# Kernel optimization log

Measured on AMD Instinct MI355X. Metric: run time of the kernel, lower is better.

The kernel has to match this reference:

```python
import jax, jax.numpy as jnp
import numpy as np

B = 65536
D = 512            # resnet18 fc.in_features
NUM_CLASSES = 512  # size of batch_centers
LEVELS = [2048, 1024, 512]


def setup_inputs() -> dict:
    key = jax.random.key(0)
    ks = jax.random.split(key, 8)
    x = jax.random.normal(ks[0], (B, D), dtype=jnp.float32)
    labels = jax.random.randint(ks[1], (B,), 0, NUM_CLASSES, dtype=jnp.int64)
    W0 = jax.random.normal(ks[2], (LEVELS[0], D), dtype=jnp.float32) * 0.02
    b0 = jnp.zeros((LEVELS[0],), dtype=jnp.float32)
    W1 = jax.random.normal(ks[3], (LEVELS[1], LEVELS[0]), dtype=jnp.float32) * 0.02
    b1 = jnp.zeros((LEVELS[1],), dtype=jnp.float32)
    W2 = jax.random.normal(ks[4], (LEVELS[2], LEVELS[1]), dtype=jnp.float32) * 0.02
    b2 = jnp.zeros((LEVELS[2],), dtype=jnp.float32)
    lambda_values = jnp.array([1e-3, 1.0, 1.0, 1.0], dtype=jnp.float32)
    return {"x": x, "W0": W0, "b0": b0, "W1": W1, "b1": b1,
            "W2": W2, "b2": b2, "lambda_values": lambda_values,
            "labels": labels}


def _cross_entropy(logits, labels):
    # mean over batch of -log p(label) (torch CrossEntropyLoss default)
    logp = jax.nn.log_softmax(logits, axis=-1)
    nll = -jnp.take_along_axis(logp, labels[:, None], axis=-1)[:, 0]
    return jnp.mean(nll)


def reference(x, W0, b0, W1, b1, W2, b2, lambda_values, labels):
    # --- per-class scatter-mean centers (vectorized segment reduce) ---
    sums = jax.ops.segment_sum(x, labels, num_segments=NUM_CLASSES)
    counts = jax.ops.segment_sum(jnp.ones((x.shape[0],), x.dtype), labels,
                                 num_segments=NUM_CLASSES)
    centers = jnp.where(counts[:, None] > 0,
                        sums / jnp.maximum(counts, 1.0)[:, None],
                        0.0)  # classes absent from batch keep zero centers
    # --- gather-diff center loss: sum_i ||x_i - c_{y_i}||^2 ---
    diff = x - centers[labels]
    center_loss = jnp.sum(diff * diff)
    # --- cascaded classification heads, CE at each level ---
    h = x
    losses = []
    for W, b in ((W0, b0), (W1, b1), (W2, b2)):
        h = h @ W.T + b
        losses.append(_cross_entropy(h, labels))
    classification_losses = jnp.stack(losses)
    return lambda_values[0] * center_loss + jnp.dot(lambda_values[1:],
                                                    classification_losses)
```

## Files before the change

### kernel.cpp

```cpp
#include <hip/hip_runtime.h>
#include <cstdint>
#include <cstddef>

using f32x4  = __attribute__((ext_vector_type(4))) float;
using i32x4v = __attribute__((ext_vector_type(4))) int;
using i32x8v = __attribute__((ext_vector_type(8))) int;

__device__ __forceinline__ unsigned char f2fp8(float f) {
  return (unsigned char)(__builtin_amdgcn_cvt_pk_fp8_f32(f, f, 0, false) & 0xff);
}

__device__ __forceinline__ float waveRed(float v) {
#pragma unroll
  for (int m = 32; m >= 1; m >>= 1) v += __shfl_xor(v, m, 64);
  return v;
}

__device__ __forceinline__ void gload16(const void* g, void* l) {
  __builtin_amdgcn_global_load_lds(
      (__attribute__((address_space(1))) uint32_t*)(uintptr_t)g,
      (__attribute__((address_space(3))) uint32_t*)(uint32_t*)l,
      16, 0, 0);
}

__global__ __launch_bounds__(256) void prep_w(
    const float4* __restrict__ W1, const float4* __restrict__ W2,
    const float4* __restrict__ W0f4, const float* __restrict__ W0,
    const float* __restrict__ b0,
    uint32_t* __restrict__ W1_8, uint32_t* __restrict__ W2_8,
    uint32_t* __restrict__ W0_8, unsigned char* __restrict__ W0t8,
    float* __restrict__ zr, int zwords, float* __restrict__ biascat) {
  __shared__ unsigned char t8[64][65];
  const int b = blockIdx.x;
  const int tid = threadIdx.x;
  if (b < 1024) {
    for (int i = b * 256 + tid; i < 524288; i += 1024 * 256) {
      float4 v = W1[i];
      int p = __builtin_amdgcn_cvt_pk_fp8_f32(v.x, v.y, 0, false);
      p = __builtin_amdgcn_cvt_pk_fp8_f32(v.z, v.w, p, true);
      W1_8[i] = (uint32_t)p;
    }
  } else if (b < 1280) {
    for (int i = (b - 1024) * 256 + tid; i < 131072; i += 256 * 256) {
      float4 v = W2[i];
      int p = __builtin_amdgcn_cvt_pk_fp8_f32(v.x, v.y, 0, false);
      p = __builtin_amdgcn_cvt_pk_fp8_f32(v.z, v.w, p, true);
      W2_8[i] = (uint32_t)p;
    }
  } else if (b < 1536) {
    for (int i = (b - 1280) * 256 + tid; i < 262144; i += 256 * 256) {
      float4 v = W0f4[i];
      int p = __builtin_amdgcn_cvt_pk_fp8_f32(v.x, v.y, 0, false);
      p = __builtin_amdgcn_cvt_pk_fp8_f32(v.z, v.w, p, true);
      W0_8[i] = (uint32_t)p;
    }
  } else if (b < 1792) {
    const int t = b - 1536;
    const int r0 = (t >> 3) * 64, c0 = (t & 7) * 64;
#pragma unroll
    for (int p = 0; p < 16; ++p) {
      const int row = p * 4 + (tid >> 6), col = tid & 63;
      t8[row][col] = f2fp8(W0[(size_t)(r0 + row) * 512 + c0 + col]);
    }
    __syncthreads();
#pragma unroll
    for (int p = 0; p < 16; ++p) {
      const int oc = p * 4 + (tid >> 6), orr = tid & 63;
      W0t8[(size_t)(c0 + oc) * 2048 + r0 + orr] = t8[orr][oc];
    }
  } else if (b < 2819) {
    const int i = (b - 1792) * 256 + tid;
    if (i < zwords) zr[i] = 0.f;
  } else {
    const int i = (b - 2819) * 256 + tid;
    if (i < 2048) biascat[i] = b0[i];
  }
}

__global__ __launch_bounds__(256) void count_k(const int* __restrict__ lab,
                                               int* __restrict__ counts, int n) {
  __shared__ int h[512];
  for (int i = threadIdx.x; i < 512; i += 256) h[i] = 0;
  __syncthreads();
  for (int i = blockIdx.x * 256 + threadIdx.x; i < n; i += gridDim.x * 256)
    atomicAdd(&h[lab[i]], 1);
  __syncthreads();
  for (int i = threadIdx.x; i < 512; i += 256) {
    int v = h[i];
    if (v) atomicAdd(&counts[i], v);
  }
}

__global__ void prefix_k(const int* __restrict__ counts, int* __restrict__ offsets,
                         int* __restrict__ cursor, int nc) {
  const int lane = threadIdx.x;
  int base = 0;
  for (int c0 = 0; c0 < nc; c0 += 64) {
    int v = counts[c0 + lane];
    int x = v;
#pragma unroll
    for (int d = 1; d < 64; d <<= 1) {
      int y = __shfl_up(x, d, 64);
      if (lane >= d) x += y;
    }
    int excl = base + x - v;
    offsets[c0 + lane] = excl;
    cursor[c0 + lane] = excl;
    base += __shfl(x, 63, 64);
  }
}

__global__ void scatter_k(const int* __restrict__ lab, int* __restrict__ cursor,
                          int* __restrict__ buckets, int n) {
  for (int i = blockIdx.x * 256 + threadIdx.x; i < n; i += gridDim.x * 256) {
    int pos = atomicAdd(&cursor[lab[i]], 1);
    buckets[pos] = i;
  }
}

__global__ __launch_bounds__(256) void csum_k(const float* __restrict__ x,
    const int* __restrict__ buckets, const int* __restrict__ offsets,
    const int* __restrict__ counts, float* __restrict__ centers) {
  const int c = blockIdx.x >> 2, q = blockIdx.x & 3;
  const int cnt = counts[c];
  if (cnt == 0) return;
  const int beg = offsets[c];
  const int lo = beg + (cnt * q) / 4, hi = beg + (cnt * (q + 1)) / 4;
  const int t = threadIdx.x;
  float sx = 0.f, sy = 0.f;
  for (int i = lo; i < hi; ++i) {
    const int row = buckets[i];
    const float2 v = ((const float2*)(x + (size_t)row * 512))[t];
    sx += v.x; sy += v.y;
  }
  if (lo < hi) {
    atomicAdd(&centers[c * 512 + 2 * t], sx);
    atomicAdd(&centers[c * 512 + 2 * t + 1], sy);
  }
}

__global__ __launch_bounds__(256) void cnorm_k(const float* __restrict__ centers,
    const int* __restrict__ counts, float* __restrict__ out) {
  const int c = blockIdx.x;
  const int cnt = counts[c];
  if (cnt == 0) return;
  const float2 v = ((const float2*)(centers + (size_t)c * 512))[threadIdx.x];
  float ssq = v.x * v.x + v.y * v.y;
  ssq = waveRed(ssq);
  __shared__ float red[4];
  if ((threadIdx.x & 63) == 0) red[threadIdx.x >> 6] = ssq;
  __syncthreads();
  if (threadIdx.x == 0)
    atomicAdd(out, (red[0] + red[1] + red[2] + red[3]) / (float)cnt);
}

__global__ __launch_bounds__(256) void matvec_k(const float* __restrict__ W,
    const float* __restrict__ vin, const float* __restrict__ badd,
    float* __restrict__ vout, int K) {
  int row = blockIdx.x;
  float s = 0.f;
  for (int k = threadIdx.x; k < K; k += 256) s += W[(size_t)row * K + k] * vin[k];
  s = waveRed(s);
  __shared__ float red[4];
  if ((threadIdx.x & 63) == 0) red[threadIdx.x >> 6] = s;
  __syncthreads();
  if (threadIdx.x == 0) vout[row] = red[0] + red[1] + red[2] + red[3] + badd[row];
}

__global__ __launch_bounds__(256) void gemm8_w(
    const unsigned char* __restrict__ A8, const unsigned char* __restrict__ B8,
    int M, int N, int K, unsigned char* __restrict__ C8,
    unsigned char* __restrict__ Ct8) {
  __shared__ __align__(16) unsigned char As[128 * 128];
  __shared__ __align__(16) unsigned char Bs[128 * 128];
  const int tid = threadIdx.x;
  const int lane = tid & 63;
  const int wave = tid >> 6;
  const int lane16 = lane & 15;
  const int quad = lane >> 4;
  const int wm = (wave >> 1) * 64;
  const int wn = (wave & 1) * 64;
  const int m0 = blockIdx.y * 128;
  const int n0 = blockIdx.x * 128;

  f32x4 acc[4][4] = {};

  int srow[4], goff[4];
#pragma unroll
  for (int q = 0; q < 4; ++q) {
    const int s = tid + q * 256;
    const int row = s >> 3;
    const int c16 = s & 7;
    srow[q] = row;
    goff[q] = (((c16 >> 1) ^ (row & 3)) << 5) + ((c16 & 1) << 4);
  }

  for (int kt = 0; kt < K; kt += 128) {
#pragma unroll
    for (int q = 0; q < 4; ++q) {
      const int s = tid + q * 256;
      gload16(A8 + (size_t)(m0 + srow[q]) * K + kt + goff[q], &As[s * 16]);
      gload16(B8 + (size_t)(n0 + srow[q]) * K + kt + goff[q], &Bs[s * 16]);
    }
    __syncthreads();
    i32x8v a8[4], b8[4];
#pragma unroll
    for (int i = 0; i < 4; ++i) {
      const int row = i * 16 + lane16;
      const int sc = quad ^ (row & 3);
      const unsigned char* pa = &As[row * 128 + sc * 32];
      const i32x4v lo = *(const i32x4v*)pa;
      const i32x4v hi = *(const i32x4v*)(pa + 16);
      a8[i] = (i32x8v){lo[0], lo[1], lo[2], lo[3], hi[0], hi[1], hi[2], hi[3]};
    }
#pragma unroll
    for (int j = 0; j < 4; ++j) {
      const int row = j * 16 + lane16;
      const int sc = quad ^ (row & 3);
      const unsigned char* pb = &Bs[row * 128 + sc * 32];
      const i32x4v lo = *(const i32x4v*)pb;
      const i32x4v hi = *(const i32x4v*)(pb + 16);
      b8[j] = (i32x8v){lo[0], lo[1], lo[2], lo[3], hi[0], hi[1], hi[2], hi[3]};
    }
#pragma unroll
    for (int i = 0; i < 4; ++i)
#pragma unroll
      for (int j = 0; j < 4; ++j)
        acc[i][j] = __builtin_amdgcn_mfma_scale_f32_16x16x128_f8f6f4(
            a8[i], b8[j], acc[i][j], 0, 0, 0, 0x7f7f7f7f, 0, 0x7f7f7f7f);
    __syncthreads();
  }
#pragma unroll
  for (int i = 0; i < 4; ++i)
#pragma unroll
    for (int r = 0; r < 4; ++r) {
      const int rowg = m0 + wm + i * 16 + quad * 4 + r;
#pragma unroll
      for (int j = 0; j < 4; ++j) {
        const int colg = n0 + wn + j * 16 + lane16;
        const unsigned char v8 = f2fp8(acc[i][j][r]);
        C8[(size_t)rowg * N + colg] = v8;
        if (Ct8) Ct8[(size_t)colg * M + rowg] = v8;
      }
    }
}

__global__ void reorder_k(const unsigned char* __restrict__ in,
                          unsigned char* __restrict__ out) {
  const int id = blockIdx.x * 256 + threadIdx.x;
  const int col = id >> 4;
  const int k32 = id & 15;
  const int kt = k32 >> 2, quad = k32 & 3;
  const size_t src = (size_t)col * 512 + k32 * 32;
  const size_t dst = (size_t)(col >> 6) * 32768 + (size_t)kt * 8192 +
                     (size_t)((col >> 4) & 3) * 2048 +
                     (size_t)(quad * 16 + (col & 15)) * 32;
  const uint4 a = *(const uint4*)(in + src);
  const uint4 b = *(const uint4*)(in + src + 16);
  *(uint4*)(out + dst) = a;
  *(uint4*)(out + dst + 16) = b;
}

__global__ __launch_bounds__(256, 1) void gemm_ce8(
    const float* __restrict__ x, const unsigned char* __restrict__ Bp,
    const float* __restrict__ bias, const int* __restrict__ labels,
    float* __restrict__ scal) {
  const int tid = threadIdx.x;
  const int lane = tid & 63;
  const int wave = tid >> 6;
  const int lane16 = lane & 15;
  const int quad = lane >> 4;
  const int m0 = blockIdx.x * 256 + wave * 64;

  i32x8v a[4][4];
  float ss = 0.f;
#pragma unroll
  for (int i = 0; i < 4; ++i) {
    const float* xr = x + (size_t)(m0 + i * 16 + lane16) * 512 + quad * 32;
#pragma unroll
    for (int kt = 0; kt < 4; ++kt) {
      const float4* p4 = (const float4*)(xr + kt * 128);
      int d[8];
#pragma unroll
      for (int p = 0; p < 8; ++p) {
        const float4 f = p4[p];
        ss += f.x * f.x + f.y * f.y + f.z * f.z + f.w * f.w;
        int w_ = __builtin_amdgcn_cvt_pk_fp8_f32(f.x, f.y, 0, false);
        w_ = __builtin_amdgcn_cvt_pk_fp8_f32(f.z, f.w, w_, true);
        d[p] = w_;
      }
      a[i][kt] = (i32x8v){d[0], d[1], d[2], d[3], d[4], d[5], d[6], d[7]};
    }
  }
  ss = waveRed(ss);
  if (lane == 0) atomicAdd(&scal[0], ss);

  int labr[16];
#pragma unroll
  for (int i = 0; i < 4; ++i)
#pragma unroll
    for (int r = 0; r < 4; ++r)
      labr[i * 4 + r] = labels[m0 + i * 16 + quad * 4 + r];

  const unsigned char* bp = Bp + lane * 32;
  i32x8v bc[4], bn[4];
#pragma unroll
  for (int j = 0; j < 4; ++j) bc[j] = *(const i32x8v*)(bp + j * 2048);
  bp += 8192;

  float es[16];
#pragma unroll
  for (int k = 0; k < 16; ++k) es[k] = 0.f;
  float pk = 0.f;

  int tile = 0;
#pragma unroll 1
  for (int lvl = 0; lvl < 3; ++lvl) {
    const int nt = (lvl == 0) ? 32 : (lvl == 1) ? 16 : 8;
    const int cbase = (lvl == 0) ? 0 : (lvl == 1) ? 2048 : 3072;
#pragma unroll 1
    for (int t = 0; t < nt; ++t, ++tile) {
      f32x4 acc[4][4] = {};
#pragma unroll
      for (int kt = 0; kt < 4; ++kt) {
#pragma unroll
        for (int j = 0; j < 4; ++j) bn[j] = *(const i32x8v*)(bp + j * 2048);
        bp += 8192;
#pragma unroll
        for (int i = 0; i < 4; ++i)
#pragma unroll
          for (int j = 0; j < 4; ++j)
            acc[i][j] = __builtin_amdgcn_mfma_scale_f32_16x16x128_f8f6f4(
                a[i][kt], bc[j], acc[i][j], 0, 0, 0, 0x7f7f7f7f, 0, 0x7f7f7f7f);
#pragma unroll
        for (int j = 0; j < 4; ++j) bc[j] = bn[j];
      }
      float bj[4];
      int colr[4];
#pragma unroll
      for (int j = 0; j < 4; ++j) {
        const int cg = tile * 64 + j * 16 + lane16;
        bj[j] = bias[cg];
        colr[j] = cg - cbase;
      }
#pragma unroll
      for (int i = 0; i < 4; ++i)
#pragma unroll
        for (int r = 0; r < 4; ++r) {
          const int lb = labr[i * 4 + r];
          float e = 0.f;
#pragma unroll
          for (int j = 0; j < 4; ++j) {
            const float v = acc[i][j][r] + bj[j];
            e += __expf(v);
            if (colr[j] == lb) pk += v;
          }
          es[i * 4 + r] += e;
        }
    }
    float ls = 0.f;
#pragma unroll
    for (int k = 0; k < 16; ++k) {
      float tot = es[k];
      tot += __shfl_xor(tot, 1, 64);
      tot += __shfl_xor(tot, 2, 64);
      tot += __shfl_xor(tot, 4, 64);
      tot += __shfl_xor(tot, 8, 64);
      if (lane16 == 0) ls += __logf(tot);
      es[k] = 0.f;
    }
    ls = waveRed(ls);
    pk = waveRed(pk);
    if (lane == 0) atomicAdd(&scal[2 + lvl], ls - pk);
    pk = 0.f;
  }
}

__global__ void fin_k(const float* __restrict__ scal, const float* __restrict__ lam,
                      float* __restrict__ out, float invB) {
  if (threadIdx.x == 0 && blockIdx.x == 0)
    out[0] = lam[0] * (scal[0] - scal[1]) +
             (lam[1] * scal[2] + lam[2] * scal[3] + lam[3] * scal[4]) * invB;
}

extern "C" void kernel_launch(void* const* d_in, const int* in_sizes, int n_in,
                              void* d_out, int out_size, void* d_ws, size_t ws_size,
                              hipStream_t stream) {
  const float* x   = (const float*)d_in[0];
  const float* W0  = (const float*)d_in[1];
  const float* b0  = (const float*)d_in[2];
  const float* W1  = (const float*)d_in[3];
  const float* b1  = (const float*)d_in[4];
  const float* W2  = (const float*)d_in[5];
  const float* b2  = (const float*)d_in[6];
  const float* lam = (const float*)d_in[7];
  const int*   lab = (const int*)d_in[8];

  const int Bsz = in_sizes[8];
  const int D   = in_sizes[0] / Bsz;
  const int N0  = in_sizes[2];
  const int N1  = in_sizes[4];
  const int N2  = in_sizes[6];
  const int Ncat = N0 + N1 + N2;
  const int NCLS = 512;

  char* w = (char*)d_ws;
  size_t off = 0;
  auto alloc = [&](size_t bytes) -> void* {
    void* p = w + off;
    off += (bytes + 255) & ~(size_t)255;
    return p;
  };

  unsigned char* Bcat8 = (unsigned char*)alloc((size_t)Ncat * D);
  unsigned char* Bp    = (unsigned char*)alloc((size_t)Ncat * D + 8192);
  unsigned char* W1_8  = (unsigned char*)alloc((size_t)N1 * N0);
  unsigned char* W2_8  = (unsigned char*)alloc((size_t)N2 * N1);
  unsigned char* W0t8  = (unsigned char*)alloc((size_t)D * N0);
  unsigned char* M1t8  = (unsigned char*)alloc((size_t)D * N1);
  float* biascat = (float*)alloc((size_t)Ncat * 4);
  int* offsets = (int*)alloc(NCLS * 4);
  int* cursor  = (int*)alloc(NCLS * 4);
  int* buckets = (int*)alloc((size_t)Bsz * 4);
  const int zwords = NCLS + 8 + NCLS * 512;
  char* zr = (char*)alloc((size_t)zwords * 4);
  int*   counts  = (int*)zr;
  float* scal    = (float*)(zr + NCLS * 4);
  float* centers = (float*)(zr + NCLS * 4 + 32);
  (void)ws_size; (void)n_in; (void)out_size;

  prep_w<<<dim3(2827), dim3(256), 0, stream>>>(
      (const float4*)W1, (const float4*)W2, (const float4*)W0, W0, b0,
      (uint32_t*)W1_8, (uint32_t*)W2_8, (uint32_t*)Bcat8, W0t8,
      (float*)zr, zwords, biascat);

  count_k<<<dim3(32), dim3(256), 0, stream>>>(lab, counts, Bsz);
  prefix_k<<<dim3(1), dim3(64), 0, stream>>>(counts, offsets, cursor, NCLS);
  scatter_k<<<dim3(256), dim3(256), 0, stream>>>(lab, cursor, buckets, Bsz);
  csum_k<<<dim3(4 * NCLS), dim3(256), 0, stream>>>(x, buckets, offsets, counts, centers);
  cnorm_k<<<dim3(NCLS), dim3(256), 0, stream>>>(centers, counts, &scal[1]);

  matvec_k<<<dim3(N1), dim3(256), 0, stream>>>(W1, b0, b1, biascat + N0, N0);
  matvec_k<<<dim3(N2), dim3(256), 0, stream>>>(W2, biascat + N0, b2, biascat + N0 + N1, N1);

  gemm8_w<<<dim3(D / 128, N1 / 128), dim3(256), 0, stream>>>(
      W1_8, W0t8, N1, D, N0, Bcat8 + (size_t)N0 * D, M1t8);
  gemm8_w<<<dim3(D / 128, N2 / 128), dim3(256), 0, stream>>>(
      W2_8, M1t8, N2, D, N1, Bcat8 + (size_t)(N0 + N1) * D, nullptr);

  reorder_k<<<dim3(Ncat * D / 32 / 256), dim3(256), 0, stream>>>(Bcat8, Bp);

  gemm_ce8<<<dim3(Bsz / 256), dim3(256), 0, stream>>>(x, Bp, biascat, lab, scal);

  fin_k<<<dim3(1), dim3(64), 0, stream>>>(scal, lam, (float*)d_out, 1.f / (float)Bsz);
}
```

Measured before the change: 488.5 us.

## Compute label-logit terms from class sums and halve GEMM-CE rows per wave

The per-row label-logit pick in the fused GEMM+CE kernel is replaced by an algebraic shortcut: the sum of picked logits equals the per-class center sums dotted with the fp8 weight rows, plus count times bias. A new small kernel computes this. The sum of squares of x moves into csum_k. gemm_ce8 now handles 32 rows per wave instead of 64, with two blocks per CU and a double-buffered B load per tile. This cuts register pressure and the compare work in the epilogue, at the cost of reading B twice as often per row.

After: 539.7 us. 10.5% more time.

```diff
diff --git a/kernel.cpp b/kernel.cpp
--- a/kernel.cpp
+++ b/kernel.cpp
@@ -8,6 +8,19 @@
 
 __device__ __forceinline__ unsigned char f2fp8(float f) {
   return (unsigned char)(__builtin_amdgcn_cvt_pk_fp8_f32(f, f, 0, false) & 0xff);
+}
+
+__device__ __forceinline__ float fp8b0(unsigned int w) {
+  return __builtin_amdgcn_cvt_f32_fp8(w, 0);
+}
+__device__ __forceinline__ float fp8b1(unsigned int w) {
+  return __builtin_amdgcn_cvt_f32_fp8(w, 1);
+}
+__device__ __forceinline__ float fp8b2(unsigned int w) {
+  return __builtin_amdgcn_cvt_f32_fp8(w, 2);
+}
+__device__ __forceinline__ float fp8b3(unsigned int w) {
+  return __builtin_amdgcn_cvt_f32_fp8(w, 3);
 }
 
 __device__ __forceinline__ float waveRed(float v) {
@@ -68,12 +81,15 @@
       const int oc = p * 4 + (tid >> 6), orr = tid & 63;
       W0t8[(size_t)(c0 + oc) * 2048 + r0 + orr] = t8[orr][oc];
     }
-  } else if (b < 2819) {
-    const int i = (b - 1792) * 256 + tid;
-    if (i < zwords) zr[i] = 0.f;
   } else {
-    const int i = (b - 2819) * 256 + tid;
-    if (i < 2048) biascat[i] = b0[i];
+    const int zb = (zwords + 255) >> 8;
+    if (b < 1792 + zb) {
+      const int i = (b - 1792) * 256 + tid;
+      if (i < zwords) zr[i] = 0.f;
+    } else {
+      const int i = (b - 1792 - zb) * 256 + tid;
+      if (i < 2048) biascat[i] = b0[i];
+    }
   }
 }
 
@@ -120,22 +136,36 @@
 
 __global__ __launch_bounds__(256) void csum_k(const float* __restrict__ x,
     const int* __restrict__ buckets, const int* __restrict__ offsets,
-    const int* __restrict__ counts, float* __restrict__ centers) {
+    const int* __restrict__ counts, float* __restrict__ centers,
+    float* __restrict__ scal) {
   const int c = blockIdx.x >> 2, q = blockIdx.x & 3;
   const int cnt = counts[c];
-  if (cnt == 0) return;
-  const int beg = offsets[c];
-  const int lo = beg + (cnt * q) / 4, hi = beg + (cnt * (q + 1)) / 4;
   const int t = threadIdx.x;
-  float sx = 0.f, sy = 0.f;
-  for (int i = lo; i < hi; ++i) {
-    const int row = buckets[i];
-    const float2 v = ((const float2*)(x + (size_t)row * 512))[t];
-    sx += v.x; sy += v.y;
-  }
-  if (lo < hi) {
-    atomicAdd(&centers[c * 512 + 2 * t], sx);
-    atomicAdd(&centers[c * 512 + 2 * t + 1], sy);
+  float sx = 0.f, sy = 0.f, ssq = 0.f;
+  int lo = 0, hi = 0;
+  if (cnt) {
+    const int beg = offsets[c];
+    lo = beg + (cnt * q) / 4;
+    hi = beg + (cnt * (q + 1)) / 4;
+    for (int i = lo; i < hi; ++i) {
+      const int row = buckets[i];
+      const float2 v = ((const float2*)(x + (size_t)row * 512))[t];
+      sx += v.x;
+      sy += v.y;
+      ssq += v.x * v.x + v.y * v.y;
+    }
+    if (lo < hi) {
+      atomicAdd(&centers[c * 512 + 2 * t], sx);
+      atomicAdd(&centers[c * 512 + 2 * t + 1], sy);
+    }
+  }
+  ssq = waveRed(ssq);
+  __shared__ float red[4];
+  if ((t & 63) == 0) red[t >> 6] = ssq;
+  __syncthreads();
+  if (t == 0) {
+    const float s = red[0] + red[1] + red[2] + red[3];
+    if (s != 0.f) atomicAdd(&scal[0], s);
   }
 }
 
@@ -165,6 +195,28 @@
   if ((threadIdx.x & 63) == 0) red[threadIdx.x >> 6] = s;
   __syncthreads();
   if (threadIdx.x == 0) vout[row] = red[0] + red[1] + red[2] + red[3] + badd[row];
+}
+
+__global__ void pk_k(const float* __restrict__ centers,
+                     const unsigned char* __restrict__ Bcat8,
+                     const float* __restrict__ biascat,
+                     const int* __restrict__ counts, float* __restrict__ scal) {
+  const int b = blockIdx.x;
+  const int lvl = b >> 9;
+  const int c = b & 511;
+  const int lane = threadIdx.x;
+  const int cbase = (lvl == 0) ? 0 : (lvl == 1) ? 2048 : 3072;
+  const float4* S = (const float4*)(centers + (size_t)c * 512);
+  const uint2 wb = ((const uint2*)(Bcat8 + (size_t)(cbase + c) * 512))[lane];
+  const float4 s0 = S[lane * 2];
+  const float4 s1 = S[lane * 2 + 1];
+  float s = s0.x * fp8b0(wb.x) + s0.y * fp8b1(wb.x) +
+            s0.z * fp8b2(wb.x) + s0.w * fp8b3(wb.x) +
+            s1.x * fp8b0(wb.y) + s1.y * fp8b1(wb.y) +
+            s1.z * fp8b2(wb.y) + s1.w * fp8b3(wb.y);
+  s = waveRed(s);
+  if (lane == 0)
+    atomicAdd(&scal[5 + lvl], s + (float)counts[c] * biascat[cbase + c]);
 }
 
 __global__ __launch_bounds__(256) void gemm8_w(
@@ -261,21 +313,19 @@
   *(uint4*)(out + dst + 16) = b;
 }
 
-__global__ __launch_bounds__(256, 1) void gemm_ce8(
+__global__ __launch_bounds__(256, 2) void gemm_ce8(
     const float* __restrict__ x, const unsigned char* __restrict__ Bp,
-    const float* __restrict__ bias, const int* __restrict__ labels,
-    float* __restrict__ scal) {
+    const float* __restrict__ bias, float* __restrict__ scal) {
   const int tid = threadIdx.x;
   const int lane = tid & 63;
   const int wave = tid >> 6;
   const int lane16 = lane & 15;
   const int quad = lane >> 4;
-  const int m0 = blockIdx.x * 256 + wave * 64;
-
-  i32x8v a[4][4];
-  float ss = 0.f;
-#pragma unroll
-  for (int i = 0; i < 4; ++i) {
+  const int m0 = blockIdx.x * 128 + wave * 32;
+
+  i32x8v a[2][4];
+#pragma unroll
+  for (int i = 0; i < 2; ++i) {
     const float* xr = x + (size_t)(m0 + i * 16 + lane16) * 512 + quad * 32;
 #pragma unroll
     for (int kt = 0; kt < 4; ++kt) {
@@ -284,7 +334,6 @@
 #pragma unroll
       for (int p = 0; p < 8; ++p) {
         const float4 f = p4[p];
-        ss += f.x * f.x + f.y * f.y + f.z * f.z + f.w * f.w;
         int w_ = __builtin_amdgcn_cvt_pk_fp8_f32(f.x, f.y, 0, false);
         w_ = __builtin_amdgcn_cvt_pk_fp8_f32(f.z, f.w, w_, true);
         d[p] = w_;
@@ -292,15 +341,6 @@
       a[i][kt] = (i32x8v){d[0], d[1], d[2], d[3], d[4], d[5], d[6], d[7]};
     }
   }
-  ss = waveRed(ss);
-  if (lane == 0) atomicAdd(&scal[0], ss);
-
-  int labr[16];
-#pragma unroll
-  for (int i = 0; i < 4; ++i)
-#pragma unroll
-    for (int r = 0; r < 4; ++r)
-      labr[i * 4 + r] = labels[m0 + i * 16 + quad * 4 + r];
 
   const unsigned char* bp = Bp + lane * 32;
   i32x8v bc[4], bn[4];
@@ -308,59 +348,57 @@
   for (int j = 0; j < 4; ++j) bc[j] = *(const i32x8v*)(bp + j * 2048);
   bp += 8192;
 
-  float es[16];
-#pragma unroll
-  for (int k = 0; k < 16; ++k) es[k] = 0.f;
-  float pk = 0.f;
+  float es[8];
+#pragma unroll
+  for (int k = 0; k < 8; ++k) es[k] = 0.f;
 
   int tile = 0;
 #pragma unroll 1
   for (int lvl = 0; lvl < 3; ++lvl) {
     const int nt = (lvl == 0) ? 32 : (lvl == 1) ? 16 : 8;
-    const int cbase = (lvl == 0) ? 0 : (lvl == 1) ? 2048 : 3072;
 #pragma unroll 1
     for (int t = 0; t < nt; ++t, ++tile) {
-      f32x4 acc[4][4] = {};
-#pragma unroll
-      for (int kt = 0; kt < 4; ++kt) {
+      f32x4 acc[2][4] = {};
+#pragma unroll
+      for (int kt2 = 0; kt2 < 2; ++kt2) {
 #pragma unroll
         for (int j = 0; j < 4; ++j) bn[j] = *(const i32x8v*)(bp + j * 2048);
         bp += 8192;
 #pragma unroll
-        for (int i = 0; i < 4; ++i)
+        for (int i = 0; i < 2; ++i)
 #pragma unroll
           for (int j = 0; j < 4; ++j)
             acc[i][j] = __builtin_amdgcn_mfma_scale_f32_16x16x128_f8f6f4(
-                a[i][kt], bc[j], acc[i][j], 0, 0, 0, 0x7f7f7f7f, 0, 0x7f7f7f7f);
-#pragma unroll
-        for (int j = 0; j < 4; ++j) bc[j] = bn[j];
+                a[i][kt2 * 2], bc[j], acc[i][j], 0, 0, 0, 0x7f7f7f7f, 0,
+                0x7f7f7f7f);
+#pragma unroll
+        for (int j = 0; j < 4; ++j) bc[j] = *(const i32x8v*)(bp + j * 2048);
+        bp += 8192;
+#pragma unroll
+        for (int i = 0; i < 2; ++i)
+#pragma unroll
+          for (int j = 0; j < 4; ++j)
+            acc[i][j] = __builtin_amdgcn_mfma_scale_f32_16x16x128_f8f6f4(
+                a[i][kt2 * 2 + 1], bn[j], acc[i][j], 0, 0, 0, 0x7f7f7f7f, 0,
+                0x7f7f7f7f);
       }
       float bj[4];
-      int colr[4];
-#pragma unroll
-      for (int j = 0; j < 4; ++j) {
-        const int cg = tile * 64 + j * 16 + lane16;
-        bj[j] = bias[cg];
-        colr[j] = cg - cbase;
-      }
-#pragma unroll
-      for (int i = 0; i < 4; ++i)
+#pragma unroll
+      for (int j = 0; j < 4; ++j) bj[j] = bias[tile * 64 + j * 16 + lane16];
+#pragma unroll
+      for (int i = 0; i < 2; ++i)
 #pragma unroll
         for (int r = 0; r < 4; ++r) {
-          const int lb = labr[i * 4 + r];
           float e = 0.f;
 #pragma unroll
-          for (int j = 0; j < 4; ++j) {
-            const float v = acc[i][j][r] + bj[j];
-            e += __expf(v);
-            if (colr[j] == lb) pk += v;
-          }
+          for (int j = 0; j < 4; ++j) e += __expf(acc[i][j][r] + bj[j]);
           es[i * 4 + r] += e;
         }
+      __builtin_amdgcn_s_barrier();
     }
     float ls = 0.f;
 #pragma unroll
-    for (int k = 0; k < 16; ++k) {
+    for (int k = 0; k < 8; ++k) {
       float tot = es[k];
       tot += __shfl_xor(tot, 1, 64);
       tot += __shfl_xor(tot, 2, 64);
@@ -370,9 +408,7 @@
       es[k] = 0.f;
     }
     ls = waveRed(ls);
-    pk = waveRed(pk);
-    if (lane == 0) atomicAdd(&scal[2 + lvl], ls - pk);
-    pk = 0.f;
+    if (lane == 0) atomicAdd(&scal[2 + lvl], ls);
   }
 }
 
@@ -380,7 +416,8 @@
                       float* __restrict__ out, float invB) {
   if (threadIdx.x == 0 && blockIdx.x == 0)
     out[0] = lam[0] * (scal[0] - scal[1]) +
-             (lam[1] * scal[2] + lam[2] * scal[3] + lam[3] * scal[4]) * invB;
+             (lam[1] * (scal[2] - scal[5]) + lam[2] * (scal[3] - scal[6]) +
+              lam[3] * (scal[4] - scal[7])) * invB;
 }
 
 extern "C" void kernel_launch(void* const* d_in, const int* in_sizes, int n_in,
@@ -413,7 +450,7 @@
   };
 
   unsigned char* Bcat8 = (unsigned char*)alloc((size_t)Ncat * D);
-  unsigned char* Bp    = (unsigned char*)alloc((size_t)Ncat * D + 8192);
+  unsigned char* Bp    = (unsigned char*)alloc((size_t)Ncat * D + 16384);
   unsigned char* W1_8  = (unsigned char*)alloc((size_t)N1 * N0);
   unsigned char* W2_8  = (unsigned char*)alloc((size_t)N2 * N1);
   unsigned char* W0t8  = (unsigned char*)alloc((size_t)D * N0);
@@ -429,7 +466,8 @@
   float* centers = (float*)(zr + NCLS * 4 + 32);
   (void)ws_size; (void)n_in; (void)out_size;
 
-  prep_w<<<dim3(2827), dim3(256), 0, stream>>>(
+  const int zb = (zwords + 255) / 256;
+  prep_w<<<dim3(1792 + zb + 8), dim3(256), 0, stream>>>(
       (const float4*)W1, (const float4*)W2, (const float4*)W0, W0, b0,
       (uint32_t*)W1_8, (uint32_t*)W2_8, (uint32_t*)Bcat8, W0t8,
       (float*)zr, zwords, biascat);
@@ -437,7 +475,8 @@
   count_k<<<dim3(32), dim3(256), 0, stream>>>(lab, counts, Bsz);
   prefix_k<<<dim3(1), dim3(64), 0, stream>>>(counts, offsets, cursor, NCLS);
   scatter_k<<<dim3(256), dim3(256), 0, stream>>>(lab, cursor, buckets, Bsz);
-  csum_k<<<dim3(4 * NCLS), dim3(256), 0, stream>>>(x, buckets, offsets, counts, centers);
+  csum_k<<<dim3(4 * NCLS), dim3(256), 0, stream>>>(x, buckets, offsets, counts,
+                                                   centers, scal);
   cnorm_k<<<dim3(NCLS), dim3(256), 0, stream>>>(centers, counts, &scal[1]);
 
   matvec_k<<<dim3(N1), dim3(256), 0, stream>>>(W1, b0, b1, biascat + N0, N0);
@@ -450,7 +489,10 @@
 
   reorder_k<<<dim3(Ncat * D / 32 / 256), dim3(256), 0, stream>>>(Bcat8, Bp);
 
-  gemm_ce8<<<dim3(Bsz / 256), dim3(256), 0, stream>>>(x, Bp, biascat, lab, scal);
+  pk_k<<<dim3(3 * NCLS), dim3(64), 0, stream>>>(centers, Bcat8, biascat,
+                                                counts, scal);
+
+  gemm_ce8<<<dim3(Bsz / 128), dim3(256), 0, stream>>>(x, Bp, biascat, scal);
 
   fin_k<<<dim3(1), dim3(64), 0, stream>>>(scal, lam, (float*)d_out, 1.f / (float)Bsz);
 }
```
